# Kernel tuning notes

Measured on AMD Instinct MI355X. Metric: run time of the kernel, lower is better.

Reference implementation:

```python
import jax, jax.numpy as jnp
import numpy as np

DIM = 1024
HEADS = 16
HEAD_DIM = DIM // HEADS


def setup_inputs() -> dict:
    key = jax.random.key(0)
    ks = jax.random.split(key, 5)
    s = 1.0 / np.sqrt(DIM)
    x = jax.random.normal(ks[0], (2, 2048, DIM), dtype=jnp.float32)
    # torch nn.Linear weights are [out_features, in_features]
    W_qkv = jax.random.uniform(ks[1], (3 * DIM, DIM), dtype=jnp.float32, minval=-s, maxval=s)
    b_qkv = jax.random.uniform(ks[2], (3 * DIM,), dtype=jnp.float32, minval=-s, maxval=s)
    W_out = jax.random.uniform(ks[3], (DIM, DIM), dtype=jnp.float32, minval=-s, maxval=s)
    b_out = jax.random.uniform(ks[4], (DIM,), dtype=jnp.float32, minval=-s, maxval=s)
    return {"x": x, "W_qkv": W_qkv, "b_qkv": b_qkv, "W_out": W_out, "b_out": b_out}


def reference(x, W_qkv, b_qkv, W_out, b_out):
    B, N, D = x.shape
    qkv = jnp.einsum('bnd,ed->bne', x, W_qkv) + b_qkv            # [B,N,3D]
    qkv = qkv.reshape(B, N, 3, HEADS, HEAD_DIM)
    qkv = jnp.transpose(qkv, (2, 0, 3, 1, 4))                    # [3,B,H,N,hd]
    q, k, v = qkv[0], qkv[1], qkv[2]
    scale = 1.0 / np.sqrt(HEAD_DIM).astype(np.float32)
    attn = jnp.einsum('bhnd,bhmd->bhnm', q, k) * scale           # [B,H,N,N]
    attn = jax.nn.softmax(attn, axis=-1)
    out = jnp.einsum('bhnm,bhmd->bhnd', attn, v)                 # [B,H,N,hd]
    out = jnp.transpose(out, (0, 2, 1, 3)).reshape(B, N, D)
    out = jnp.einsum('bnd,ed->bne', out, W_out) + b_out
    return out
```

## Files before the change

### kernel.cpp

```cpp
#include <hip/hip_runtime.h>
#include <stdint.h>
#include <stddef.h>

typedef __attribute__((ext_vector_type(4))) float  f32x4;
typedef __attribute__((ext_vector_type(8))) short  s16x8;
typedef __attribute__((ext_vector_type(4))) float  float4v;
typedef __attribute__((ext_vector_type(4))) unsigned short u16x4;
typedef __attribute__((ext_vector_type(2))) unsigned int   u32x2;

#define DIM    1024
#define HEADS  16
#define HD     64
#define SEQ    2048
#define BATCH  2
#define TOKENS (BATCH * SEQ)

#define QSCALE 0.18033688011112042f

__device__ __forceinline__ unsigned short f2bf(float f) {
  union { float f; uint32_t u; } x; x.f = f;
  uint32_t r = x.u + 0x7fffu + ((x.u >> 16) & 1u);
  return (unsigned short)(r >> 16);
}

__device__ __forceinline__ float fast_exp2(float x) {
#if __has_builtin(__builtin_amdgcn_exp2f)
  return __builtin_amdgcn_exp2f(x);
#else
  return exp2f(x);
#endif
}

__device__ __forceinline__ uint32_t pack_bf16_trunc(uint32_t lo, uint32_t hi) {
#if __has_builtin(__builtin_amdgcn_perm)
  return __builtin_amdgcn_perm(hi, lo, 0x07060302u);
#else
  return (hi & 0xffff0000u) | (lo >> 16);
#endif
}

__device__ __forceinline__ void stage16(const unsigned short* gp, unsigned short* lp) {
#if __has_builtin(__builtin_amdgcn_global_load_lds)
  __builtin_amdgcn_global_load_lds((const __attribute__((address_space(1))) void*)gp,
                                   (__attribute__((address_space(3))) void*)lp, 16, 0, 0);
#else
  *(s16x8*)(lp + (threadIdx.x & 63) * 8) = *(const s16x8*)gp;
#endif
}

#define N4_X  (TOKENS * DIM / 4)
#define N4_WQ (3 * DIM * DIM / 4)
#define N4_WO (DIM * DIM / 4)
__global__ __launch_bounds__(256) void mhsa_cast_all(const float* __restrict__ x,
    const float* __restrict__ wq, const float* __restrict__ wo,
    unsigned short* __restrict__ xb, unsigned short* __restrict__ wqb,
    unsigned short* __restrict__ wob) {
  int i = blockIdx.x * 256 + threadIdx.x;
  const float* src; unsigned short* dst; int off;
  if (i < N4_X)              { src = x;  dst = xb;  off = i; }
  else if (i < N4_X + N4_WQ) { src = wq; dst = wqb; off = i - N4_X; }
  else                       { src = wo; dst = wob; off = i - (N4_X + N4_WQ); }
  float4v f = ((const float4v*)src)[off];
  u16x4 o;
  o.x = f2bf(f.x); o.y = f2bf(f.y); o.z = f2bf(f.z); o.w = f2bf(f.w);
  ((u16x4*)dst)[off] = o;
}


__global__ __launch_bounds__(256, 3) void mhsa_gemm_qkv(const unsigned short* __restrict__ A,
    const unsigned short* __restrict__ Bw, const float* __restrict__ bias,
    unsigned short* __restrict__ qws, unsigned short* __restrict__ kws,
    unsigned short* __restrict__ vws) {
  __shared__ unsigned short As[2][128 * 32];
  __shared__ unsigned short Bs[2][128 * 32];
  const int t = threadIdx.x;
  const int w = t >> 6, l = t & 63;
  const int wm = w >> 1, wn = w & 1;
  const int rowBase = blockIdx.y * 128;
  const int colBase = blockIdx.x * 128;
  const int fr = l & 15, q4 = l >> 4, ln = l & 15;
  const int srow = l >> 2;
  const int scol = ((l & 3) ^ (srow & 3)) * 8;

  f32x4 zero = {0.f, 0.f, 0.f, 0.f};
  f32x4 acc[4][4];
  #pragma unroll
  for (int a = 0; a < 4; ++a)
    #pragma unroll
    for (int b = 0; b < 4; ++b) acc[a][b] = zero;

  #pragma unroll
  for (int it = 0; it < 2; ++it) {
    const int c = w * 2 + it;
    stage16(A  + (size_t)(rowBase + c * 16 + srow) * DIM + scol, &As[0][c * 512]);
    stage16(Bw + (size_t)(colBase + c * 16 + srow) * DIM + scol, &Bs[0][c * 512]);
  }
  __syncthreads();

  for (int kt = 0; kt < DIM / 32; ++kt) {
    const int cur = kt & 1, nxt = cur ^ 1;
    if (kt + 1 < DIM / 32) {
      const int k1 = (kt + 1) * 32;
      #pragma unroll
      for (int it = 0; it < 2; ++it) {
        const int c = w * 2 + it;
        stage16(A  + (size_t)(rowBase + c * 16 + srow) * DIM + k1 + scol, &As[nxt][c * 512]);
        stage16(Bw + (size_t)(colBase + c * 16 + srow) * DIM + k1 + scol, &Bs[nxt][c * 512]);
      }
    }
    s16x8 xf[4], wf[4];
    #pragma unroll
    for (int b = 0; b < 4; ++b)
      xf[b] = *(const s16x8*)&As[cur][(wm * 64 + b * 16 + fr) * 32 + ((q4 ^ (fr & 3)) * 8)];
    #pragma unroll
    for (int a = 0; a < 4; ++a)
      wf[a] = *(const s16x8*)&Bs[cur][(wn * 64 + a * 16 + fr) * 32 + ((q4 ^ (fr & 3)) * 8)];
    #pragma unroll
    for (int a = 0; a < 4; ++a)
      #pragma unroll
      for (int b = 0; b < 4; ++b)
        acc[a][b] = __builtin_amdgcn_mfma_f32_16x16x32_bf16(wf[a], xf[b], acc[a][b], 0, 0, 0);
    __syncthreads();
  }

  const int which = colBase >> 10;
  const float sc = (which == 0) ? QSCALE : 1.0f;
  unsigned short* dst = (which == 0) ? qws : ((which == 1) ? kws : vws);

  #pragma unroll
  for (int a = 0; a < 4; ++a) {
    const int e0 = colBase + wn * 64 + a * 16 + q4 * 4;
    const float4v bs4 = *(const float4v*)&bias[e0];
    const int rr0 = e0 & 1023;
    const int h = rr0 >> 6, d0 = rr0 & 63;
    #pragma unroll
    for (int b = 0; b < 4; ++b) {
      const int tok = rowBase + wm * 64 + b * 16 + ln;
      const int bb = tok >> 11, n = tok & 2047;
      if (which != 2) {
        u16x4 pk;
        #pragma unroll
        for (int r = 0; r < 4; ++r) pk[r] = f2bf((acc[a][b][r] + bs4[r]) * sc);
        *(u16x4*)&dst[(((size_t)(bb * HEADS + h)) * SEQ + n) * HD + d0] = pk;
      } else {
        #pragma unroll
        for (int r = 0; r < 4; ++r)
          dst[(((size_t)(bb * HEADS + h)) * HD + d0 + r) * SEQ + n] =
              f2bf(acc[a][b][r] + bs4[r]);
      }
    }
  }
}

__global__ __launch_bounds__(256, 3) void mhsa_gemm_out(const unsigned short* __restrict__ A,
    const unsigned short* __restrict__ Bw, const float* __restrict__ bias,
    float* __restrict__ out) {
  __shared__ unsigned short As[2][64 * 32];
  __shared__ unsigned short Bs[2][128 * 32];
  const int t = threadIdx.x;
  const int w = t >> 6, l = t & 63;
  const int wm = w >> 1, wn = w & 1;
  const int rowBase = blockIdx.y * 64;
  const int colBase = blockIdx.x * 128;
  const int fr = l & 15, q4 = l >> 4, ln = l & 15;
  const int srow = l >> 2;
  const int scol = ((l & 3) ^ (srow & 3)) * 8;

  f32x4 zero = {0.f, 0.f, 0.f, 0.f};
  f32x4 acc[4][2];
  #pragma unroll
  for (int a = 0; a < 4; ++a)
    #pragma unroll
    for (int b = 0; b < 2; ++b) acc[a][b] = zero;

  #pragma unroll
  for (int it = 0; it < 3; ++it) {
    const int s = w * 3 + it;
    if (s < 4) stage16(A  + (size_t)(rowBase + s * 16 + srow) * DIM + scol, &As[0][s * 512]);
    else       stage16(Bw + (size_t)(colBase + (s - 4) * 16 + srow) * DIM + scol, &Bs[0][(s - 4) * 512]);
  }
  __syncthreads();

  for (int kt = 0; kt < DIM / 32; ++kt) {
    const int cur = kt & 1, nxt = cur ^ 1;
    if (kt + 1 < DIM / 32) {
      const int k1 = (kt + 1) * 32;
      #pragma unroll
      for (int it = 0; it < 3; ++it) {
        const int s = w * 3 + it;
        if (s < 4) stage16(A  + (size_t)(rowBase + s * 16 + srow) * DIM + k1 + scol, &As[nxt][s * 512]);
        else       stage16(Bw + (size_t)(colBase + (s - 4) * 16 + srow) * DIM + k1 + scol, &Bs[nxt][(s - 4) * 512]);
      }
    }
    s16x8 xf[2], wf[4];
    #pragma unroll
    for (int b = 0; b < 2; ++b)
      xf[b] = *(const s16x8*)&As[cur][(wm * 32 + b * 16 + fr) * 32 + ((q4 ^ (fr & 3)) * 8)];
    #pragma unroll
    for (int a = 0; a < 4; ++a)
      wf[a] = *(const s16x8*)&Bs[cur][(wn * 64 + a * 16 + fr) * 32 + ((q4 ^ (fr & 3)) * 8)];
    #pragma unroll
    for (int a = 0; a < 4; ++a)
      #pragma unroll
      for (int b = 0; b < 2; ++b)
        acc[a][b] = __builtin_amdgcn_mfma_f32_16x16x32_bf16(wf[a], xf[b], acc[a][b], 0, 0, 0);
    __syncthreads();
  }

  #pragma unroll
  for (int a = 0; a < 4; ++a) {
    const int e0 = colBase + wn * 64 + a * 16 + q4 * 4;
    const float4v bs4 = *(const float4v*)&bias[e0];
    #pragma unroll
    for (int b = 0; b < 2; ++b) {
      const int tok = rowBase + wm * 32 + b * 16 + ln;
      float4v v;
      #pragma unroll
      for (int r = 0; r < 4; ++r) v[r] = acc[a][b][r] + bs4[r];
      *(float4v*)&out[(size_t)tok * DIM + e0] = v;
    }
  }
}

__global__ __launch_bounds__(256, 2) void mhsa_attn(const unsigned short* __restrict__ q,
    const unsigned short* __restrict__ k, const unsigned short* __restrict__ vt,
    unsigned short* __restrict__ o) {
  __shared__ unsigned short QPs[4 * 32 * 72];
  __shared__ unsigned short Ks[2][64 * 64];
  __shared__ unsigned short Vs[2][64 * 64];
  const int t = threadIdx.x, w = t >> 6, l = t & 63;
  const int q4 = l >> 4, ln = l & 15;
  const int bh = blockIdx.y, q0 = blockIdx.x * 128;
  const unsigned short* qb  = q  + (size_t)bh * SEQ * HD;
  const unsigned short* kb  = k  + (size_t)bh * SEQ * HD;
  const unsigned short* vtb = vt + (size_t)bh * HD * SEQ;

  const int srow = l >> 3;
  const int scol = ((l & 7) ^ srow) * 8;

  unsigned short* Pw = &QPs[w * (32 * 72)];

  const s16x8 vones = {(short)0x3F80, (short)0x3F80, (short)0x3F80, (short)0x3F80,
                       (short)0x3F80, (short)0x3F80, (short)0x3F80, (short)0x3F80};

  #pragma unroll
  for (int it = 0; it < 4; ++it)
    stage16(qb + (size_t)(q0 + w * 32 + it * 8 + srow) * HD + scol, &Pw[it * 512]);
  #pragma unroll
  for (int it = 0; it < 2; ++it) {
    const int c = w + it * 4;
    stage16(kb  + (size_t)(c * 8 + srow) * HD + scol,        &Ks[0][c * 512]);
    stage16(vtb + (size_t)(c * 8 + srow) * SEQ + scol,       &Vs[0][c * 512]);
    stage16(kb  + (size_t)(64 + c * 8 + srow) * HD + scol,   &Ks[1][c * 512]);
  }
  __syncthreads();

  s16x8 aq[2][2];
  #pragma unroll
  for (int i = 0; i < 2; ++i)
    #pragma unroll
    for (int kk = 0; kk < 2; ++kk)
      aq[i][kk] = *(const s16x8*)&Pw[(i * 16 + ln) * 64 + (((kk * 4 + q4) ^ (ln & 7)) * 8)];

  f32x4 zero = {0.f, 0.f, 0.f, 0.f};
  f32x4 accO[2][4];
  f32x4 accS[2] = {zero, zero};
  #pragma unroll
  for (int i = 0; i < 2; ++i)
    #pragma unroll
    for (int jd = 0; jd < 4; ++jd) accO[i][jd] = zero;

  {
    f32x4 St[4][2];
    #pragma unroll
    for (int jb = 0; jb < 4; ++jb)
      #pragma unroll
      for (int i = 0; i < 2; ++i) St[jb][i] = zero;
    __builtin_amdgcn_s_setprio(1);
    #pragma unroll
    for (int jb = 0; jb < 4; ++jb) {
      s16x8 ak0 = *(const s16x8*)&Ks[0][(jb * 16 + ln) * 64 + ((q4 ^ (ln & 7)) * 8)];
      s16x8 ak1 = *(const s16x8*)&Ks[0][(jb * 16 + ln) * 64 + (((4 + q4) ^ (ln & 7)) * 8)];
      #pragma unroll
      for (int i = 0; i < 2; ++i) {
        St[jb][i] = __builtin_amdgcn_mfma_f32_16x16x32_bf16(ak0, aq[i][0], St[jb][i], 0, 0, 0);
        St[jb][i] = __builtin_amdgcn_mfma_f32_16x16x32_bf16(ak1, aq[i][1], St[jb][i], 0, 0, 0);
      }
    }
    __builtin_amdgcn_s_setprio(0);
    #pragma unroll
    for (int i = 0; i < 2; ++i)
      #pragma unroll
      for (int jb = 0; jb < 4; ++jb) {
        uint32_t u0 = __float_as_uint(fast_exp2(St[jb][i][0]));
        uint32_t u1 = __float_as_uint(fast_exp2(St[jb][i][1]));
        uint32_t u2 = __float_as_uint(fast_exp2(St[jb][i][2]));
        uint32_t u3 = __float_as_uint(fast_exp2(St[jb][i][3]));
        u32x2 pk;
        pk.x = pack_bf16_trunc(u0, u1);
        pk.y = pack_bf16_trunc(u2, u3);
        *(u32x2*)&Pw[(i * 16 + ln) * 72 + jb * 16 + q4 * 4] = pk;
      }
  }
  __syncthreads();

  const int NT = SEQ / 64;
  for (int jt = 0; jt < NT; ++jt) {
    const int cur = jt & 1, nxt = cur ^ 1;
    if (jt + 2 < NT) {
      const int j2 = (jt + 2) * 64;
      #pragma unroll
      for (int it = 0; it < 2; ++it) {
        const int c = w + it * 4;
        stage16(kb + (size_t)(j2 + c * 8 + srow) * HD + scol, &Ks[cur][c * 512]);
      }
    }
    if (jt + 1 < NT) {
      const int j1 = (jt + 1) * 64;
      #pragma unroll
      for (int it = 0; it < 2; ++it) {
        const int c = w + it * 4;
        stage16(vtb + (size_t)(c * 8 + srow) * SEQ + j1 + scol, &Vs[nxt][c * 512]);
      }
    }

    s16x8 ap[2][2];
    #pragma unroll
    for (int i = 0; i < 2; ++i)
      #pragma unroll
      for (int kk = 0; kk < 2; ++kk)
        ap[i][kk] = *(const s16x8*)&Pw[(i * 16 + ln) * 72 + kk * 32 + q4 * 8];

    __builtin_amdgcn_s_setprio(1);
    #pragma unroll
    for (int i = 0; i < 2; ++i) {
      accS[i] = __builtin_amdgcn_mfma_f32_16x16x32_bf16(ap[i][0], vones, accS[i], 0, 0, 0);
      accS[i] = __builtin_amdgcn_mfma_f32_16x16x32_bf16(ap[i][1], vones, accS[i], 0, 0, 0);
    }
    __builtin_amdgcn_s_setprio(0);

    if (jt + 1 < NT) {
      f32x4 St[4][2];
      #pragma unroll
      for (int jb = 0; jb < 4; ++jb)
        #pragma unroll
        for (int i = 0; i < 2; ++i) St[jb][i] = zero;
      __builtin_amdgcn_s_setprio(1);
      #pragma unroll
      for (int jb = 0; jb < 4; ++jb) {
        s16x8 ak0 = *(const s16x8*)&Ks[nxt][(jb * 16 + ln) * 64 + ((q4 ^ (ln & 7)) * 8)];
        s16x8 ak1 = *(const s16x8*)&Ks[nxt][(jb * 16 + ln) * 64 + (((4 + q4) ^ (ln & 7)) * 8)];
        #pragma unroll
        for (int i = 0; i < 2; ++i) {
          St[jb][i] = __builtin_amdgcn_mfma_f32_16x16x32_bf16(ak0, aq[i][0], St[jb][i], 0, 0, 0);
          St[jb][i] = __builtin_amdgcn_mfma_f32_16x16x32_bf16(ak1, aq[i][1], St[jb][i], 0, 0, 0);
        }
      }

      #pragma unroll
      for (int jd = 0; jd < 4; ++jd) {
        s16x8 bv0 = *(const s16x8*)&Vs[cur][(jd * 16 + ln) * 64 + ((q4 ^ (ln & 7)) * 8)];
        s16x8 bv1 = *(const s16x8*)&Vs[cur][(jd * 16 + ln) * 64 + (((4 + q4) ^ (ln & 7)) * 8)];
        #pragma unroll
        for (int i = 0; i < 2; ++i) {
          accO[i][jd] = __builtin_amdgcn_mfma_f32_16x16x32_bf16(ap[i][0], bv0, accO[i][jd], 0, 0, 0);
          accO[i][jd] = __builtin_amdgcn_mfma_f32_16x16x32_bf16(ap[i][1], bv1, accO[i][jd], 0, 0, 0);
        }
      }
      __builtin_amdgcn_s_setprio(0);

      #pragma unroll
      for (int i = 0; i < 2; ++i)
        #pragma unroll
        for (int jb = 0; jb < 4; ++jb) {
          uint32_t u0 = __float_as_uint(fast_exp2(St[jb][i][0]));
          uint32_t u1 = __float_as_uint(fast_exp2(St[jb][i][1]));
          uint32_t u2 = __float_as_uint(fast_exp2(St[jb][i][2]));
          uint32_t u3 = __float_as_uint(fast_exp2(St[jb][i][3]));
          u32x2 pk;
          pk.x = pack_bf16_trunc(u0, u1);
          pk.y = pack_bf16_trunc(u2, u3);
          *(u32x2*)&Pw[(i * 16 + ln) * 72 + jb * 16 + q4 * 4] = pk;
        }
    } else {
      __builtin_amdgcn_s_setprio(1);
      #pragma unroll
      for (int jd = 0; jd < 4; ++jd) {
        s16x8 bv0 = *(const s16x8*)&Vs[cur][(jd * 16 + ln) * 64 + ((q4 ^ (ln & 7)) * 8)];
        s16x8 bv1 = *(const s16x8*)&Vs[cur][(jd * 16 + ln) * 64 + (((4 + q4) ^ (ln & 7)) * 8)];
        #pragma unroll
        for (int i = 0; i < 2; ++i) {
          accO[i][jd] = __builtin_amdgcn_mfma_f32_16x16x32_bf16(ap[i][0], bv0, accO[i][jd], 0, 0, 0);
          accO[i][jd] = __builtin_amdgcn_mfma_f32_16x16x32_bf16(ap[i][1], bv1, accO[i][jd], 0, 0, 0);
        }
      }
      __builtin_amdgcn_s_setprio(0);
    }

    __syncthreads();
  }

  const int b = bh >> 4, h = bh & 15;
  #pragma unroll
  for (int i = 0; i < 2; ++i) {
    #pragma unroll
    for (int r = 0; r < 4; ++r) {
      const float invr = 1.f / accS[i][r];
      const int row = q0 + w * 32 + i * 16 + q4 * 4 + r;
      #pragma unroll
      for (int jd = 0; jd < 4; ++jd)
        o[((size_t)(b * SEQ + row)) * DIM + h * HD + jd * 16 + ln] = f2bf(accO[i][jd][r] * invr);
    }
  }
}

extern "C" void kernel_launch(void* const* d_in, const int* in_sizes, int n_in,
                              void* d_out, int out_size, void* d_ws, size_t ws_size,
                              hipStream_t stream) {
  const float* x     = (const float*)d_in[0];
  const float* Wqkv  = (const float*)d_in[1];
  const float* bqkv  = (const float*)d_in[2];
  const float* Wout  = (const float*)d_in[3];
  const float* bout  = (const float*)d_in[4];
  float* out = (float*)d_out;

  unsigned short* ws = (unsigned short*)d_ws;
  unsigned short* x_bf    = ws;
  unsigned short* wqkv_bf = x_bf    + (size_t)TOKENS * DIM;
  unsigned short* wout_bf = wqkv_bf + (size_t)3 * DIM * DIM;
  unsigned short* q_ws    = wout_bf + (size_t)DIM * DIM;
  unsigned short* k_ws    = q_ws    + (size_t)TOKENS * DIM;
  unsigned short* v_ws    = k_ws    + (size_t)TOKENS * DIM;
  unsigned short* ao_ws   = v_ws    + (size_t)TOKENS * DIM;

  {
    const int n4 = N4_X + N4_WQ + N4_WO;
    mhsa_cast_all<<<n4 / 256, 256, 0, stream>>>(x, Wqkv, Wout, x_bf, wqkv_bf, wout_bf);
  }

  {
    dim3 grid(3 * DIM / 128, TOKENS / 128);
    mhsa_gemm_qkv<<<grid, 256, 0, stream>>>(x_bf, wqkv_bf, bqkv, q_ws, k_ws, v_ws);
  }

  {
    dim3 grid(SEQ / 128, BATCH * HEADS);
    mhsa_attn<<<grid, 256, 0, stream>>>(q_ws, k_ws, v_ws, ao_ws);
  }

  {
    dim3 grid(DIM / 128, TOKENS / 64);
    mhsa_gemm_out<<<grid, 256, 0, stream>>>(ao_ws, wout_bf, bout, out);
  }
}
```

Baseline: 186.0 us.

## Load K/V MFMA fragments directly from global into registers, drop LDS staging

Each wave now loads its K and V^T MFMA operand fragments straight from global memory into registers, prefetching one tile ahead. The shared-memory K/V double buffers and the per-iteration block barriers are removed. This cuts LDS traffic and synchronisation. In exchange every wave (4 per block) redundantly fetches the same K/V tiles from global/L2, uses more registers for the prefetched fragments, and exposes global latency more directly.

New measurement: 261.2 us. 40.4% more time.

```diff
diff --git a/kernel.cpp b/kernel.cpp
--- a/kernel.cpp
+++ b/kernel.cpp
@@ -226,8 +226,6 @@
     const unsigned short* __restrict__ k, const unsigned short* __restrict__ vt,
     unsigned short* __restrict__ o) {
   __shared__ unsigned short QPs[4 * 32 * 72];
-  __shared__ unsigned short Ks[2][64 * 64];
-  __shared__ unsigned short Vs[2][64 * 64];
   const int t = threadIdx.x, w = t >> 6, l = t & 63;
   const int q4 = l >> 4, ln = l & 15;
   const int bh = blockIdx.y, q0 = blockIdx.x * 128;
@@ -246,13 +244,22 @@
   #pragma unroll
   for (int it = 0; it < 4; ++it)
     stage16(qb + (size_t)(q0 + w * 32 + it * 8 + srow) * HD + scol, &Pw[it * 512]);
-  #pragma unroll
-  for (int it = 0; it < 2; ++it) {
-    const int c = w + it * 4;
-    stage16(kb  + (size_t)(c * 8 + srow) * HD + scol,        &Ks[0][c * 512]);
-    stage16(vtb + (size_t)(c * 8 + srow) * SEQ + scol,       &Vs[0][c * 512]);
-    stage16(kb  + (size_t)(64 + c * 8 + srow) * HD + scol,   &Ks[1][c * 512]);
-  }
+
+  const unsigned short* kL = kb  + (size_t)ln * HD  + q4 * 8;
+  const unsigned short* vL = vtb + (size_t)ln * SEQ + q4 * 8;
+
+  s16x8 kf[4][2], vf[4][2];
+  #pragma unroll
+  for (int jb = 0; jb < 4; ++jb)
+    #pragma unroll
+    for (int kk = 0; kk < 2; ++kk)
+      kf[jb][kk] = *(const s16x8*)(kL + (size_t)jb * 16 * HD + kk * 32);
+  #pragma unroll
+  for (int jd = 0; jd < 4; ++jd)
+    #pragma unroll
+    for (int kk = 0; kk < 2; ++kk)
+      vf[jd][kk] = *(const s16x8*)(vL + (size_t)jd * 16 * SEQ + kk * 32);
+
   __syncthreads();
 
   s16x8 aq[2][2];
@@ -279,15 +286,18 @@
     __builtin_amdgcn_s_setprio(1);
     #pragma unroll
     for (int jb = 0; jb < 4; ++jb) {
-      s16x8 ak0 = *(const s16x8*)&Ks[0][(jb * 16 + ln) * 64 + ((q4 ^ (ln & 7)) * 8)];
-      s16x8 ak1 = *(const s16x8*)&Ks[0][(jb * 16 + ln) * 64 + (((4 + q4) ^ (ln & 7)) * 8)];
       #pragma unroll
       for (int i = 0; i < 2; ++i) {
-        St[jb][i] = __builtin_amdgcn_mfma_f32_16x16x32_bf16(ak0, aq[i][0], St[jb][i], 0, 0, 0);
-        St[jb][i] = __builtin_amdgcn_mfma_f32_16x16x32_bf16(ak1, aq[i][1], St[jb][i], 0, 0, 0);
+        St[jb][i] = __builtin_amdgcn_mfma_f32_16x16x32_bf16(kf[jb][0], aq[i][0], St[jb][i], 0, 0, 0);
+        St[jb][i] = __builtin_amdgcn_mfma_f32_16x16x32_bf16(kf[jb][1], aq[i][1], St[jb][i], 0, 0, 0);
       }
     }
     __builtin_amdgcn_s_setprio(0);
+    #pragma unroll
+    for (int jb = 0; jb < 4; ++jb)
+      #pragma unroll
+      for (int kk = 0; kk < 2; ++kk)
+        kf[jb][kk] = *(const s16x8*)(kL + (size_t)(64 + jb * 16) * HD + kk * 32);
     #pragma unroll
     for (int i = 0; i < 2; ++i)
       #pragma unroll
@@ -302,28 +312,9 @@
         *(u32x2*)&Pw[(i * 16 + ln) * 72 + jb * 16 + q4 * 4] = pk;
       }
   }
-  __syncthreads();
 
   const int NT = SEQ / 64;
   for (int jt = 0; jt < NT; ++jt) {
-    const int cur = jt & 1, nxt = cur ^ 1;
-    if (jt + 2 < NT) {
-      const int j2 = (jt + 2) * 64;
-      #pragma unroll
-      for (int it = 0; it < 2; ++it) {
-        const int c = w + it * 4;
-        stage16(kb + (size_t)(j2 + c * 8 + srow) * HD + scol, &Ks[cur][c * 512]);
-      }
-    }
-    if (jt + 1 < NT) {
-      const int j1 = (jt + 1) * 64;
-      #pragma unroll
-      for (int it = 0; it < 2; ++it) {
-        const int c = w + it * 4;
-        stage16(vtb + (size_t)(c * 8 + srow) * SEQ + j1 + scol, &Vs[nxt][c * 512]);
-      }
-    }
-
     s16x8 ap[2][2];
     #pragma unroll
     for (int i = 0; i < 2; ++i)
@@ -348,26 +339,39 @@
       __builtin_amdgcn_s_setprio(1);
       #pragma unroll
       for (int jb = 0; jb < 4; ++jb) {
-        s16x8 ak0 = *(const s16x8*)&Ks[nxt][(jb * 16 + ln) * 64 + ((q4 ^ (ln & 7)) * 8)];
-        s16x8 ak1 = *(const s16x8*)&Ks[nxt][(jb * 16 + ln) * 64 + (((4 + q4) ^ (ln & 7)) * 8)];
         #pragma unroll
         for (int i = 0; i < 2; ++i) {
-          St[jb][i] = __builtin_amdgcn_mfma_f32_16x16x32_bf16(ak0, aq[i][0], St[jb][i], 0, 0, 0);
-          St[jb][i] = __builtin_amdgcn_mfma_f32_16x16x32_bf16(ak1, aq[i][1], St[jb][i], 0, 0, 0);
+          St[jb][i] = __builtin_amdgcn_mfma_f32_16x16x32_bf16(kf[jb][0], aq[i][0], St[jb][i], 0, 0, 0);
+          St[jb][i] = __builtin_amdgcn_mfma_f32_16x16x32_bf16(kf[jb][1], aq[i][1], St[jb][i], 0, 0, 0);
         }
       }
 
       #pragma unroll
       for (int jd = 0; jd < 4; ++jd) {
-        s16x8 bv0 = *(const s16x8*)&Vs[cur][(jd * 16 + ln) * 64 + ((q4 ^ (ln & 7)) * 8)];
-        s16x8 bv1 = *(const s16x8*)&Vs[cur][(jd * 16 + ln) * 64 + (((4 + q4) ^ (ln & 7)) * 8)];
         #pragma unroll
         for (int i = 0; i < 2; ++i) {
-          accO[i][jd] = __builtin_amdgcn_mfma_f32_16x16x32_bf16(ap[i][0], bv0, accO[i][jd], 0, 0, 0);
-          accO[i][jd] = __builtin_amdgcn_mfma_f32_16x16x32_bf16(ap[i][1], bv1, accO[i][jd], 0, 0, 0);
+          accO[i][jd] = __builtin_amdgcn_mfma_f32_16x16x32_bf16(ap[i][0], vf[jd][0], accO[i][jd], 0, 0, 0);
+          accO[i][jd] = __builtin_amdgcn_mfma_f32_16x16x32_bf16(ap[i][1], vf[jd][1], accO[i][jd], 0, 0, 0);
         }
       }
       __builtin_amdgcn_s_setprio(0);
+
+      if (jt + 2 < NT) {
+        const unsigned short* kp = kL + (size_t)((jt + 2) * 64) * HD;
+        #pragma unroll
+        for (int jb = 0; jb < 4; ++jb)
+          #pragma unroll
+          for (int kk = 0; kk < 2; ++kk)
+            kf[jb][kk] = *(const s16x8*)(kp + (size_t)jb * 16 * HD + kk * 32);
+      }
+      {
+        const unsigned short* vp = vL + (jt + 1) * 64;
+        #pragma unroll
+        for (int jd = 0; jd < 4; ++jd)
+          #pragma unroll
+          for (int kk = 0; kk < 2; ++kk)
+            vf[jd][kk] = *(const s16x8*)(vp + (size_t)jd * 16 * SEQ + kk * 32);
+      }
 
       #pragma unroll
       for (int i = 0; i < 2; ++i)
@@ -386,18 +390,14 @@
       __builtin_amdgcn_s_setprio(1);
       #pragma unroll
       for (int jd = 0; jd < 4; ++jd) {
-        s16x8 bv0 = *(const s16x8*)&Vs[cur][(jd * 16 + ln) * 64 + ((q4 ^ (ln & 7)) * 8)];
-        s16x8 bv1 = *(const s16x8*)&Vs[cur][(jd * 16 + ln) * 64 + (((4 + q4) ^ (ln & 7)) * 8)];
         #pragma unroll
         for (int i = 0; i < 2; ++i) {
-          accO[i][jd] = __builtin_amdgcn_mfma_f32_16x16x32_bf16(ap[i][0], bv0, accO[i][jd], 0, 0, 0);
-          accO[i][jd] = __builtin_amdgcn_mfma_f32_16x16x32_bf16(ap[i][1], bv1, accO[i][jd], 0, 0, 0);
+          accO[i][jd] = __builtin_amdgcn_mfma_f32_16x16x32_bf16(ap[i][0], vf[jd][0], accO[i][jd], 0, 0, 0);
+          accO[i][jd] = __builtin_amdgcn_mfma_f32_16x16x32_bf16(ap[i][1], vf[jd][1], accO[i][jd], 0, 0, 0);
         }
       }
       __builtin_amdgcn_s_setprio(0);
     }
-
-    __syncthreads();
   }
 
   const int b = bh >> 4, h = bh & 15;
```

## Switch attention to 32x32x16 MFMA with register-resident P via permlane32 swap

Applied to the files above, without the earlier changes.

Rewrites the attention inner loop to use 32x32x16 bf16 MFMAs. The exponentiated scores are kept in registers and rearranged into the A-operand layout with v_permlane32_swap, so they no longer round-trip through an LDS P buffer. The K prefetch distance drops from two tiles to one, and the one-tile software skew between QK^T and PV is removed, so both now run in the same iteration. This cuts LDS traffic and instruction count, but it exposes the exp latency between the two matmuls and reduces how far ahead loads are issued.

Result: slower. 191.1 us (+2.7%).

```diff
diff --git a/kernel.cpp b/kernel.cpp
--- a/kernel.cpp
+++ b/kernel.cpp
@@ -2,11 +2,12 @@
 #include <stdint.h>
 #include <stddef.h>
 
-typedef __attribute__((ext_vector_type(4))) float  f32x4;
-typedef __attribute__((ext_vector_type(8))) short  s16x8;
-typedef __attribute__((ext_vector_type(4))) float  float4v;
-typedef __attribute__((ext_vector_type(4))) unsigned short u16x4;
-typedef __attribute__((ext_vector_type(2))) unsigned int   u32x2;
+typedef __attribute__((ext_vector_type(4)))  float  f32x4;
+typedef __attribute__((ext_vector_type(16))) float  f32x16;
+typedef __attribute__((ext_vector_type(8)))  short  s16x8;
+typedef __attribute__((ext_vector_type(4)))  float  float4v;
+typedef __attribute__((ext_vector_type(4)))  unsigned short u16x4;
+typedef __attribute__((ext_vector_type(4)))  unsigned int   u32x4;
 
 #define DIM    1024
 #define HEADS  16
@@ -225,11 +226,11 @@
 __global__ __launch_bounds__(256, 2) void mhsa_attn(const unsigned short* __restrict__ q,
     const unsigned short* __restrict__ k, const unsigned short* __restrict__ vt,
     unsigned short* __restrict__ o) {
-  __shared__ unsigned short QPs[4 * 32 * 72];
+  __shared__ unsigned short Qs[4][32 * 64];
   __shared__ unsigned short Ks[2][64 * 64];
   __shared__ unsigned short Vs[2][64 * 64];
   const int t = threadIdx.x, w = t >> 6, l = t & 63;
-  const int q4 = l >> 4, ln = l & 15;
+  const int ln = l & 31, hi = l >> 5;
   const int bh = blockIdx.y, q0 = blockIdx.x * 128;
   const unsigned short* qb  = q  + (size_t)bh * SEQ * HD;
   const unsigned short* kb  = k  + (size_t)bh * SEQ * HD;
@@ -237,180 +238,103 @@
 
   const int srow = l >> 3;
   const int scol = ((l & 7) ^ srow) * 8;
-
-  unsigned short* Pw = &QPs[w * (32 * 72)];
+  const int swz = ln & 7;
 
   const s16x8 vones = {(short)0x3F80, (short)0x3F80, (short)0x3F80, (short)0x3F80,
                        (short)0x3F80, (short)0x3F80, (short)0x3F80, (short)0x3F80};
 
   #pragma unroll
   for (int it = 0; it < 4; ++it)
-    stage16(qb + (size_t)(q0 + w * 32 + it * 8 + srow) * HD + scol, &Pw[it * 512]);
+    stage16(qb + (size_t)(q0 + w * 32 + it * 8 + srow) * HD + scol, &Qs[w][it * 512]);
   #pragma unroll
   for (int it = 0; it < 2; ++it) {
     const int c = w + it * 4;
-    stage16(kb  + (size_t)(c * 8 + srow) * HD + scol,        &Ks[0][c * 512]);
-    stage16(vtb + (size_t)(c * 8 + srow) * SEQ + scol,       &Vs[0][c * 512]);
-    stage16(kb  + (size_t)(64 + c * 8 + srow) * HD + scol,   &Ks[1][c * 512]);
+    stage16(kb  + (size_t)(c * 8 + srow) * HD + scol,  &Ks[0][c * 512]);
+    stage16(vtb + (size_t)(c * 8 + srow) * SEQ + scol, &Vs[0][c * 512]);
   }
   __syncthreads();
 
-  s16x8 aq[2][2];
-  #pragma unroll
-  for (int i = 0; i < 2; ++i)
-    #pragma unroll
-    for (int kk = 0; kk < 2; ++kk)
-      aq[i][kk] = *(const s16x8*)&Pw[(i * 16 + ln) * 64 + (((kk * 4 + q4) ^ (ln & 7)) * 8)];
-
-  f32x4 zero = {0.f, 0.f, 0.f, 0.f};
-  f32x4 accO[2][4];
-  f32x4 accS[2] = {zero, zero};
-  #pragma unroll
-  for (int i = 0; i < 2; ++i)
-    #pragma unroll
-    for (int jd = 0; jd < 4; ++jd) accO[i][jd] = zero;
-
-  {
-    f32x4 St[4][2];
-    #pragma unroll
-    for (int jb = 0; jb < 4; ++jb)
-      #pragma unroll
-      for (int i = 0; i < 2; ++i) St[jb][i] = zero;
-    __builtin_amdgcn_s_setprio(1);
-    #pragma unroll
-    for (int jb = 0; jb < 4; ++jb) {
-      s16x8 ak0 = *(const s16x8*)&Ks[0][(jb * 16 + ln) * 64 + ((q4 ^ (ln & 7)) * 8)];
-      s16x8 ak1 = *(const s16x8*)&Ks[0][(jb * 16 + ln) * 64 + (((4 + q4) ^ (ln & 7)) * 8)];
-      #pragma unroll
-      for (int i = 0; i < 2; ++i) {
-        St[jb][i] = __builtin_amdgcn_mfma_f32_16x16x32_bf16(ak0, aq[i][0], St[jb][i], 0, 0, 0);
-        St[jb][i] = __builtin_amdgcn_mfma_f32_16x16x32_bf16(ak1, aq[i][1], St[jb][i], 0, 0, 0);
-      }
-    }
-    __builtin_amdgcn_s_setprio(0);
-    #pragma unroll
-    for (int i = 0; i < 2; ++i)
-      #pragma unroll
-      for (int jb = 0; jb < 4; ++jb) {
-        uint32_t u0 = __float_as_uint(fast_exp2(St[jb][i][0]));
-        uint32_t u1 = __float_as_uint(fast_exp2(St[jb][i][1]));
-        uint32_t u2 = __float_as_uint(fast_exp2(St[jb][i][2]));
-        uint32_t u3 = __float_as_uint(fast_exp2(St[jb][i][3]));
-        u32x2 pk;
-        pk.x = pack_bf16_trunc(u0, u1);
-        pk.y = pack_bf16_trunc(u2, u3);
-        *(u32x2*)&Pw[(i * 16 + ln) * 72 + jb * 16 + q4 * 4] = pk;
-      }
-  }
-  __syncthreads();
+  s16x8 aq[4];
+  #pragma unroll
+  for (int kc = 0; kc < 4; ++kc)
+    aq[kc] = *(const s16x8*)&Qs[w][ln * 64 + (((2 * kc + hi) ^ swz) * 8)];
+
+  f32x16 z16;
+  #pragma unroll
+  for (int i = 0; i < 16; ++i) z16[i] = 0.f;
+  f32x16 accO0 = z16, accO1 = z16, accS = z16;
 
   const int NT = SEQ / 64;
   for (int jt = 0; jt < NT; ++jt) {
     const int cur = jt & 1, nxt = cur ^ 1;
-    if (jt + 2 < NT) {
-      const int j2 = (jt + 2) * 64;
+    if (jt + 1 < NT) {
+      const int j1 = (jt + 1) * 64;
       #pragma unroll
       for (int it = 0; it < 2; ++it) {
         const int c = w + it * 4;
-        stage16(kb + (size_t)(j2 + c * 8 + srow) * HD + scol, &Ks[cur][c * 512]);
-      }
-    }
-    if (jt + 1 < NT) {
-      const int j1 = (jt + 1) * 64;
-      #pragma unroll
-      for (int it = 0; it < 2; ++it) {
-        const int c = w + it * 4;
+        stage16(kb  + (size_t)(j1 + c * 8 + srow) * HD + scol,  &Ks[nxt][c * 512]);
         stage16(vtb + (size_t)(c * 8 + srow) * SEQ + j1 + scol, &Vs[nxt][c * 512]);
       }
     }
 
-    s16x8 ap[2][2];
-    #pragma unroll
-    for (int i = 0; i < 2; ++i)
-      #pragma unroll
-      for (int kk = 0; kk < 2; ++kk)
-        ap[i][kk] = *(const s16x8*)&Pw[(i * 16 + ln) * 72 + kk * 32 + q4 * 8];
-
+    f32x16 St0 = z16, St1 = z16;
     __builtin_amdgcn_s_setprio(1);
     #pragma unroll
-    for (int i = 0; i < 2; ++i) {
-      accS[i] = __builtin_amdgcn_mfma_f32_16x16x32_bf16(ap[i][0], vones, accS[i], 0, 0, 0);
-      accS[i] = __builtin_amdgcn_mfma_f32_16x16x32_bf16(ap[i][1], vones, accS[i], 0, 0, 0);
+    for (int kc = 0; kc < 4; ++kc) {
+      s16x8 ak0 = *(const s16x8*)&Ks[cur][ln * 64 + (((2 * kc + hi) ^ swz) * 8)];
+      s16x8 ak1 = *(const s16x8*)&Ks[cur][(32 + ln) * 64 + (((2 * kc + hi) ^ swz) * 8)];
+      St0 = __builtin_amdgcn_mfma_f32_32x32x16_bf16(ak0, aq[kc], St0, 0, 0, 0);
+      St1 = __builtin_amdgcn_mfma_f32_32x32x16_bf16(ak1, aq[kc], St1, 0, 0, 0);
     }
     __builtin_amdgcn_s_setprio(0);
 
-    if (jt + 1 < NT) {
-      f32x4 St[4][2];
-      #pragma unroll
-      for (int jb = 0; jb < 4; ++jb)
-        #pragma unroll
-        for (int i = 0; i < 2; ++i) St[jb][i] = zero;
-      __builtin_amdgcn_s_setprio(1);
-      #pragma unroll
-      for (int jb = 0; jb < 4; ++jb) {
-        s16x8 ak0 = *(const s16x8*)&Ks[nxt][(jb * 16 + ln) * 64 + ((q4 ^ (ln & 7)) * 8)];
-        s16x8 ak1 = *(const s16x8*)&Ks[nxt][(jb * 16 + ln) * 64 + (((4 + q4) ^ (ln & 7)) * 8)];
-        #pragma unroll
-        for (int i = 0; i < 2; ++i) {
-          St[jb][i] = __builtin_amdgcn_mfma_f32_16x16x32_bf16(ak0, aq[i][0], St[jb][i], 0, 0, 0);
-          St[jb][i] = __builtin_amdgcn_mfma_f32_16x16x32_bf16(ak1, aq[i][1], St[jb][i], 0, 0, 0);
-        }
-      }
-
-      #pragma unroll
-      for (int jd = 0; jd < 4; ++jd) {
-        s16x8 bv0 = *(const s16x8*)&Vs[cur][(jd * 16 + ln) * 64 + ((q4 ^ (ln & 7)) * 8)];
-        s16x8 bv1 = *(const s16x8*)&Vs[cur][(jd * 16 + ln) * 64 + (((4 + q4) ^ (ln & 7)) * 8)];
-        #pragma unroll
-        for (int i = 0; i < 2; ++i) {
-          accO[i][jd] = __builtin_amdgcn_mfma_f32_16x16x32_bf16(ap[i][0], bv0, accO[i][jd], 0, 0, 0);
-          accO[i][jd] = __builtin_amdgcn_mfma_f32_16x16x32_bf16(ap[i][1], bv1, accO[i][jd], 0, 0, 0);
-        }
-      }
-      __builtin_amdgcn_s_setprio(0);
-
-      #pragma unroll
-      for (int i = 0; i < 2; ++i)
-        #pragma unroll
-        for (int jb = 0; jb < 4; ++jb) {
-          uint32_t u0 = __float_as_uint(fast_exp2(St[jb][i][0]));
-          uint32_t u1 = __float_as_uint(fast_exp2(St[jb][i][1]));
-          uint32_t u2 = __float_as_uint(fast_exp2(St[jb][i][2]));
-          uint32_t u3 = __float_as_uint(fast_exp2(St[jb][i][3]));
-          u32x2 pk;
-          pk.x = pack_bf16_trunc(u0, u1);
-          pk.y = pack_bf16_trunc(u2, u3);
-          *(u32x2*)&Pw[(i * 16 + ln) * 72 + jb * 16 + q4 * 4] = pk;
-        }
-    } else {
-      __builtin_amdgcn_s_setprio(1);
-      #pragma unroll
-      for (int jd = 0; jd < 4; ++jd) {
-        s16x8 bv0 = *(const s16x8*)&Vs[cur][(jd * 16 + ln) * 64 + ((q4 ^ (ln & 7)) * 8)];
-        s16x8 bv1 = *(const s16x8*)&Vs[cur][(jd * 16 + ln) * 64 + (((4 + q4) ^ (ln & 7)) * 8)];
-        #pragma unroll
-        for (int i = 0; i < 2; ++i) {
-          accO[i][jd] = __builtin_amdgcn_mfma_f32_16x16x32_bf16(ap[i][0], bv0, accO[i][jd], 0, 0, 0);
-          accO[i][jd] = __builtin_amdgcn_mfma_f32_16x16x32_bf16(ap[i][1], bv1, accO[i][jd], 0, 0, 0);
-        }
-      }
-      __builtin_amdgcn_s_setprio(0);
-    }
+    uint32_t cp0[8], cp1[8];
+    #pragma unroll
+    for (int m = 0; m < 8; ++m) {
+      cp0[m] = pack_bf16_trunc(__float_as_uint(fast_exp2(St0[2 * m])),
+                               __float_as_uint(fast_exp2(St0[2 * m + 1])));
+      cp1[m] = pack_bf16_trunc(__float_as_uint(fast_exp2(St1[2 * m])),
+                               __float_as_uint(fast_exp2(St1[2 * m + 1])));
+    }
+
+    s16x8 pa[4];
+    #pragma unroll
+    for (int ks = 0; ks < 4; ++ks) {
+      const int tb = 4 * (ks & 1);
+      uint32_t d0 = (ks < 2) ? cp0[tb + 0] : cp1[tb + 0];
+      uint32_t d1 = (ks < 2) ? cp0[tb + 1] : cp1[tb + 1];
+      uint32_t d2 = (ks < 2) ? cp0[tb + 2] : cp1[tb + 2];
+      uint32_t d3 = (ks < 2) ? cp0[tb + 3] : cp1[tb + 3];
+      asm("v_permlane32_swap_b32 %0, %1" : "+v"(d0), "+v"(d2));
+      asm("v_permlane32_swap_b32 %0, %1" : "+v"(d1), "+v"(d3));
+      u32x4 pd; pd.x = d0; pd.y = d1; pd.z = d2; pd.w = d3;
+      pa[ks] = __builtin_bit_cast(s16x8, pd);
+    }
+
+    __builtin_amdgcn_s_setprio(1);
+    #pragma unroll
+    for (int ks = 0; ks < 4; ++ks)
+      accS = __builtin_amdgcn_mfma_f32_32x32x16_bf16(pa[ks], vones, accS, 0, 0, 0);
+    #pragma unroll
+    for (int ks = 0; ks < 4; ++ks) {
+      s16x8 bv0 = *(const s16x8*)&Vs[cur][ln * 64 + (((2 * ks + hi) ^ swz) * 8)];
+      s16x8 bv1 = *(const s16x8*)&Vs[cur][(32 + ln) * 64 + (((2 * ks + hi) ^ swz) * 8)];
+      accO0 = __builtin_amdgcn_mfma_f32_32x32x16_bf16(pa[ks], bv0, accO0, 0, 0, 0);
+      accO1 = __builtin_amdgcn_mfma_f32_32x32x16_bf16(pa[ks], bv1, accO1, 0, 0, 0);
+    }
+    __builtin_amdgcn_s_setprio(0);
 
     __syncthreads();
   }
 
   const int b = bh >> 4, h = bh & 15;
   #pragma unroll
-  for (int i = 0; i < 2; ++i) {
-    #pragma unroll
-    for (int r = 0; r < 4; ++r) {
-      const float invr = 1.f / accS[i][r];
-      const int row = q0 + w * 32 + i * 16 + q4 * 4 + r;
-      #pragma unroll
-      for (int jd = 0; jd < 4; ++jd)
-        o[((size_t)(b * SEQ + row)) * DIM + h * HD + jd * 16 + ln] = f2bf(accO[i][jd][r] * invr);
-    }
+  for (int r = 0; r < 16; ++r) {
+    const int ql = (r & 3) + 8 * (r >> 2) + 4 * hi;
+    const float inv = 1.f / accS[r];
+    const int row = q0 + w * 32 + ql;
+    o[((size_t)(b * SEQ + row)) * DIM + h * HD + ln]      = f2bf(accO0[r] * inv);
+    o[((size_t)(b * SEQ + row)) * DIM + h * HD + 32 + ln] = f2bf(accO1[r] * inv);
   }
 }
 
```
